# Kernel optimization log

Measured on AMD Instinct MI355X. Metric: run time of the kernel, lower is better.

Reference implementation:

```python
import jax, jax.numpy as jnp
import numpy as np
from jax import lax

N_BLOCK = 4  # unfold kernel/stride

SOBEL_X = jnp.array([[-1., 0., 1.], [-2., 0., 2.], [-1., 0., 1.]], dtype=jnp.float32)
SOBEL_Y = jnp.array([[-1., -2., -1.], [0., 0., 0.], [1., 2., 1.]], dtype=jnp.float32)


def setup_inputs() -> dict:
    key = jax.random.key(0)
    k1, k2 = jax.random.split(key)
    output = jax.random.normal(k1, (16, 1, 1024, 1024), dtype=jnp.float32)
    target = jax.random.normal(k2, (16, 1, 1024, 1024), dtype=jnp.float32)
    return {"output": output, "target": target}


def _sobel(img, kernel):
    # img: (B,1,H,W); cross-correlation with padding 1 (matches nn.Conv2d)
    return lax.conv_general_dilated(img, kernel[None, None], (1, 1), ((1, 1), (1, 1)))


def _block_var(g, n):
    # g: (B,1,H,W) -> per non-overlapping n x n block variance (unbiased=False)
    B, _, H, W = g.shape
    blocks = g.reshape(B, H // n, n, W // n, n)
    m = blocks.mean(axis=(2, 4))
    m2 = (blocks * blocks).mean(axis=(2, 4))
    return (m2 - m * m).reshape(B, -1)  # (B, (H//n)*(W//n))


def reference(output, target):
    loss = jnp.float32(0.0)
    for kern in (SOBEL_X, SOBEL_Y):
        var_out = _block_var(_sobel(output, kern), N_BLOCK)
        var_tgt = _block_var(_sobel(target, kern), N_BLOCK)
        d = var_out - var_tgt
        loss = loss + jnp.sum(d * d)  # MSELoss(reduction='sum')
    return loss
```

## Files before the change

### kernel.cpp

```cpp
#include <hip/hip_runtime.h>

#define IMG_H 1024
#define IMG_W 1024


struct RowRegs { float4 ma, mb; float la, ra_, lb, rb_; };
struct HAB { float hA[4]; float hB[4]; };

__global__ __launch_bounds__(256) void gvl_main(const float* __restrict__ A,
                                                const float* __restrict__ B,
                                                float* __restrict__ partial) {
    const int t    = threadIdx.x;
    const int wave = (blockIdx.x << 2) | (t >> 6);
    const int lane = t & 63;
    const int img   = wave >> 8;
    const int rem   = wave & 255;
    const int band  = rem >> 2;
    const int strip = rem & 3;
    const int y0    = band << 4;
    const int col0  = (strip << 8) | (lane << 2);

    const float* __restrict__ Ab = A + (size_t)img * (IMG_H * IMG_W);
    const float* __restrict__ Bb = B + (size_t)img * (IMG_H * IMG_W);

    const float mlc = (col0 > 0) ? 1.f : 0.f;
    const float mrc = (col0 + 4 < IMG_W) ? 1.f : 0.f;
    const int xl = (col0 > 0) ? col0 - 1 : 0;
    const int xr = (col0 + 4 < IMG_W) ? col0 + 4 : IMG_W - 1;
    const float zlast = (band == 63) ? 0.f : 1.f;

    auto load_row = [&](int y, RowRegs& R) {
        int yc = y < IMG_H ? y : IMG_H - 1;
        const float* ra = Ab + (size_t)yc * IMG_W;
        const float* rb = Bb + (size_t)yc * IMG_W;
        R.ma  = *reinterpret_cast<const float4*>(ra + col0);
        R.la  = ra[xl];  R.ra_ = ra[xr];
        R.mb  = *reinterpret_cast<const float4*>(rb + col0);
        R.lb  = rb[xl];  R.rb_ = rb[xr];
    };
    auto load_group = [&](RowRegs (&S)[4], int ys) {
#pragma unroll
        for (int r = 0; r < 4; ++r) load_row(ys + r, S[r]);
    };

    auto mk = [&](const float4 m, float l, float r, HAB& o) {
        float w0 = l * mlc, w5 = r * mrc;
        o.hA[0] = m.y - w0;  o.hA[1] = m.z - m.x;
        o.hA[2] = m.w - m.y; o.hA[3] = w5 - m.z;
        o.hB[0] = w0 + 2.f * m.x + m.y;
        o.hB[1] = m.x + 2.f * m.y + m.z;
        o.hB[2] = m.y + 2.f * m.z + m.w;
        o.hB[3] = m.z + 2.f * m.w + w5;
    };

    HAB a2, a1, b2, b1;
    float loss = 0.f;

    auto emit = [&](const HAB& p2, const HAB& p1, const HAB& p0,
                    float& sX, float& sX2, float& sY, float& sY2) {
#pragma unroll
        for (int c = 0; c < 4; ++c) {
            float gx = p2.hA[c] + 2.f * p1.hA[c] + p0.hA[c];
            float gy = p0.hB[c] - p2.hB[c];
            sX += gx; sX2 += gx * gx;
            sY += gy; sY2 += gy * gy;
        }
    };

    auto do_group = [&](const RowRegs (&S)[4], float rm3) {
        float sXa = 0.f, sX2a = 0.f, sYa = 0.f, sY2a = 0.f;
        float sXb = 0.f, sX2b = 0.f, sYb = 0.f, sY2b = 0.f;
#pragma unroll
        for (int r = 0; r < 4; ++r) {
            HAB a0, b0;
            mk(S[r].ma, S[r].la, S[r].ra_, a0);
            mk(S[r].mb, S[r].lb, S[r].rb_, b0);
            if (r == 3) {
#pragma unroll
                for (int c = 0; c < 4; ++c) {
                    a0.hA[c] *= rm3; a0.hB[c] *= rm3;
                    b0.hA[c] *= rm3; b0.hB[c] *= rm3;
                }
            }
            emit(a2, a1, a0, sXa, sX2a, sYa, sY2a);
            emit(b2, b1, b0, sXb, sX2b, sYb, sY2b);
            a2 = a1; a1 = a0; b2 = b1; b1 = b0;
        }
        float mXa = sXa * 0.0625f, mYa = sYa * 0.0625f;
        float vXa = sX2a * 0.0625f - mXa * mXa;
        float vYa = sY2a * 0.0625f - mYa * mYa;
        float mXb = sXb * 0.0625f, mYb = sYb * 0.0625f;
        float vXb = sX2b * 0.0625f - mXb * mXb;
        float vYb = sY2b * 0.0625f - mYb * mYb;
        float dX = vXa - vXb, dY = vYa - vYb;
        loss += dX * dX + dY * dY;
    };

    RowRegs P0, P1, N[4], M[4];
    const bool hasPrev = (band > 0);
    if (hasPrev) load_row(y0 - 1, P0);
    load_row(y0, P1);
    load_group(N, y0 + 1);
    if (hasPrev) {
        mk(P0.ma, P0.la, P0.ra_, a2);
        mk(P0.mb, P0.lb, P0.rb_, b2);
    } else {
#pragma unroll
        for (int c = 0; c < 4; ++c) { a2.hA[c] = a2.hB[c] = 0.f; b2.hA[c] = b2.hB[c] = 0.f; }
    }
    mk(P1.ma, P1.la, P1.ra_, a1);
    mk(P1.mb, P1.lb, P1.rb_, b1);

#pragma unroll
    for (int i = 0; i < 2; ++i) {
        load_group(M, y0 + 8 * i + 5);
        do_group(N, 1.f);
        if (i < 1) load_group(N, y0 + 8 * i + 9);
        do_group(M, (i == 1) ? zlast : 1.f);
    }

#pragma unroll
    for (int off = 32; off > 0; off >>= 1) loss += __shfl_down(loss, off);
    if (lane == 0) partial[wave] = loss;
}

__global__ __launch_bounds__(256) void gvl_final(const float* __restrict__ partial,
                                                 float* __restrict__ out) {
    int t = threadIdx.x;
    float s = 0.f;
#pragma unroll
    for (int i = 0; i < 16; ++i) s += partial[t + (i << 8)];
#pragma unroll
    for (int off = 32; off > 0; off >>= 1) s += __shfl_down(s, off);
    __shared__ float ws[4];
    if ((t & 63) == 0) ws[t >> 6] = s;
    __syncthreads();
    if (t == 0) out[0] = ws[0] + ws[1] + ws[2] + ws[3];
}

extern "C" void kernel_launch(void* const* d_in, const int* in_sizes, int n_in,
                              void* d_out, int out_size, void* d_ws, size_t ws_size,
                              hipStream_t stream) {
    const float* out_img = (const float*)d_in[0];
    const float* tgt_img = (const float*)d_in[1];
    float* partial = (float*)d_ws;
    gvl_main<<<1024, 256, 0, stream>>>(out_img, tgt_img, partial);
    gvl_final<<<1, 256, 0, stream>>>(partial, (float*)d_out);
}
```

Baseline: 30.06 us.

## Use 8-column lanes with shuffle halos and 8-row bands with double-buffered rows

```diff
diff --git a/kernel.cpp b/kernel.cpp
--- a/kernel.cpp
+++ b/kernel.cpp
@@ -4,8 +4,7 @@
 #define IMG_W 1024
 
 
-struct RowRegs { float4 ma, mb; float la, ra_, lb, rb_; };
-struct HAB { float hA[4]; float hB[4]; };
+struct Row { float4 qa0, qa1, qb0, qb1; float ea, eb; };
 
 __global__ __launch_bounds__(256) void gvl_main(const float* __restrict__ A,
                                                 const float* __restrict__ B,
@@ -15,108 +14,114 @@
     const int lane = t & 63;
     const int img   = wave >> 8;
     const int rem   = wave & 255;
-    const int band  = rem >> 2;
-    const int strip = rem & 3;
-    const int y0    = band << 4;
-    const int col0  = (strip << 8) | (lane << 2);
+    const int band  = rem >> 1;
+    const int strip = rem & 1;
+    const int y0    = band << 3;
+    const int c0    = (strip << 9) | (lane << 3);
+    const int ecol  = strip ? 511 : 512;
 
-    const float* __restrict__ Ab = A + (size_t)img * (IMG_H * IMG_W);
-    const float* __restrict__ Bb = B + (size_t)img * (IMG_H * IMG_W);
+    const float* __restrict__ Ab = A + (size_t)img * (size_t)(IMG_H * IMG_W);
+    const float* __restrict__ Bb = B + (size_t)img * (size_t)(IMG_H * IMG_W);
 
-    const float mlc = (col0 > 0) ? 1.f : 0.f;
-    const float mrc = (col0 + 4 < IMG_W) ? 1.f : 0.f;
-    const int xl = (col0 > 0) ? col0 - 1 : 0;
-    const int xr = (col0 + 4 < IMG_W) ? col0 + 4 : IMG_W - 1;
-    const float zlast = (band == 63) ? 0.f : 1.f;
+    const float eLs = strip ? 1.f : 0.f;
+    const float eRs = strip ? 0.f : 1.f;
+    const float maskPrev = (band > 0)    ? 1.f : 0.f;
+    const float zlast    = (band == 127) ? 0.f : 1.f;
 
-    auto load_row = [&](int y, RowRegs& R) {
-        int yc = y < IMG_H ? y : IMG_H - 1;
+    auto load_row = [&](int y, Row& R) {
+        int yc = y < 0 ? 0 : (y > IMG_H - 1 ? IMG_H - 1 : y);
         const float* ra = Ab + (size_t)yc * IMG_W;
         const float* rb = Bb + (size_t)yc * IMG_W;
-        R.ma  = *reinterpret_cast<const float4*>(ra + col0);
-        R.la  = ra[xl];  R.ra_ = ra[xr];
-        R.mb  = *reinterpret_cast<const float4*>(rb + col0);
-        R.lb  = rb[xl];  R.rb_ = rb[xr];
-    };
-    auto load_group = [&](RowRegs (&S)[4], int ys) {
-#pragma unroll
-        for (int r = 0; r < 4; ++r) load_row(ys + r, S[r]);
+        R.qa0 = *reinterpret_cast<const float4*>(ra + c0);
+        R.qa1 = *reinterpret_cast<const float4*>(ra + c0 + 4);
+        R.qb0 = *reinterpret_cast<const float4*>(rb + c0);
+        R.qb1 = *reinterpret_cast<const float4*>(rb + c0 + 4);
+        R.ea  = ra[ecol];
+        R.eb  = rb[ecol];
     };
 
-    auto mk = [&](const float4 m, float l, float r, HAB& o) {
-        float w0 = l * mlc, w5 = r * mrc;
-        o.hA[0] = m.y - w0;  o.hA[1] = m.z - m.x;
-        o.hA[2] = m.w - m.y; o.hA[3] = w5 - m.z;
-        o.hB[0] = w0 + 2.f * m.x + m.y;
-        o.hB[1] = m.x + 2.f * m.y + m.z;
-        o.hB[2] = m.y + 2.f * m.z + m.w;
-        o.hB[3] = m.z + 2.f * m.w + w5;
-    };
+    float aX2[8], aX1[8], aB2[8], aB1[8];
+    float bX2[8], bX1[8], bB2[8], bB1[8];
+    float sX[2][2], sXX[2][2], sY[2][2], sYY[2][2];
+#pragma unroll
+    for (int i = 0; i < 2; ++i)
+#pragma unroll
+        for (int j = 0; j < 2; ++j) { sX[i][j] = sXX[i][j] = sY[i][j] = sYY[i][j] = 0.f; }
 
-    HAB a2, a1, b2, b1;
-    float loss = 0.f;
-
-    auto emit = [&](const HAB& p2, const HAB& p1, const HAB& p0,
-                    float& sX, float& sX2, float& sY, float& sY2) {
+    auto calc_h = [&](const float4 q0, const float4 q1, float e, float m,
+                      float (&hX)[8], float (&hB)[8]) {
+        float lv = __shfl_up(q1.w, 1);
+        float rv = __shfl_down(q0.x, 1);
+        lv = (lane == 0)  ? e * eLs : lv;
+        rv = (lane == 63) ? e * eRs : rv;
+        float w[10] = {lv, q0.x, q0.y, q0.z, q0.w, q1.x, q1.y, q1.z, q1.w, rv};
 #pragma unroll
-        for (int c = 0; c < 4; ++c) {
-            float gx = p2.hA[c] + 2.f * p1.hA[c] + p0.hA[c];
-            float gy = p0.hB[c] - p2.hB[c];
-            sX += gx; sX2 += gx * gx;
-            sY += gy; sY2 += gy * gy;
+        for (int c = 0; c < 8; ++c) {
+            hX[c] = (w[c + 2] - w[c]) * m;
+            hB[c] = (w[c] + 2.f * w[c + 1] + w[c + 2]) * m;
         }
     };
 
-    auto do_group = [&](const RowRegs (&S)[4], float rm3) {
-        float sXa = 0.f, sX2a = 0.f, sYa = 0.f, sY2a = 0.f;
-        float sXb = 0.f, sX2b = 0.f, sYb = 0.f, sY2b = 0.f;
+    auto proc_img = [&](const float4 q0, const float4 q1, float e, float m,
+                        float (&X2)[8], float (&X1)[8], float (&B2)[8], float (&B1)[8],
+                        float (&sXi)[2], float (&sXXi)[2],
+                        float (&sYi)[2], float (&sYYi)[2]) {
+        float lv = __shfl_up(q1.w, 1);
+        float rv = __shfl_down(q0.x, 1);
+        lv = (lane == 0)  ? e * eLs : lv;
+        rv = (lane == 63) ? e * eRs : rv;
+        float w[10] = {lv, q0.x, q0.y, q0.z, q0.w, q1.x, q1.y, q1.z, q1.w, rv};
 #pragma unroll
-        for (int r = 0; r < 4; ++r) {
-            HAB a0, b0;
-            mk(S[r].ma, S[r].la, S[r].ra_, a0);
-            mk(S[r].mb, S[r].lb, S[r].rb_, b0);
-            if (r == 3) {
-#pragma unroll
-                for (int c = 0; c < 4; ++c) {
-                    a0.hA[c] *= rm3; a0.hB[c] *= rm3;
-                    b0.hA[c] *= rm3; b0.hB[c] *= rm3;
-                }
-            }
-            emit(a2, a1, a0, sXa, sX2a, sYa, sY2a);
-            emit(b2, b1, b0, sXb, sX2b, sYb, sY2b);
-            a2 = a1; a1 = a0; b2 = b1; b1 = b0;
+        for (int c = 0; c < 8; ++c) {
+            float hX = (w[c + 2] - w[c]) * m;
+            float hB = (w[c] + 2.f * w[c + 1] + w[c + 2]) * m;
+            float gx = X2[c] + 2.f * X1[c] + hX;
+            float gy = hB - B2[c];
+            const int blk = c >> 2;
+            sXi[blk] += gx;  sXXi[blk] += gx * gx;
+            sYi[blk] += gy;  sYYi[blk] += gy * gy;
+            X2[c] = X1[c];  X1[c] = hX;
+            B2[c] = B1[c];  B1[c] = hB;
         }
-        float mXa = sXa * 0.0625f, mYa = sYa * 0.0625f;
-        float vXa = sX2a * 0.0625f - mXa * mXa;
-        float vYa = sY2a * 0.0625f - mYa * mYa;
-        float mXb = sXb * 0.0625f, mYb = sYb * 0.0625f;
-        float vXb = sX2b * 0.0625f - mXb * mXb;
-        float vYb = sY2b * 0.0625f - mYb * mYb;
-        float dX = vXa - vXb, dY = vYa - vYb;
-        loss += dX * dX + dY * dY;
     };
 
-    RowRegs P0, P1, N[4], M[4];
-    const bool hasPrev = (band > 0);
-    if (hasPrev) load_row(y0 - 1, P0);
-    load_row(y0, P1);
-    load_group(N, y0 + 1);
-    if (hasPrev) {
-        mk(P0.ma, P0.la, P0.ra_, a2);
-        mk(P0.mb, P0.lb, P0.rb_, b2);
-    } else {
+    float loss = 0.f;
+    auto finalize = [&]() {
 #pragma unroll
-        for (int c = 0; c < 4; ++c) { a2.hA[c] = a2.hB[c] = 0.f; b2.hA[c] = b2.hB[c] = 0.f; }
-    }
-    mk(P1.ma, P1.la, P1.ra_, a1);
-    mk(P1.mb, P1.lb, P1.rb_, b1);
+        for (int j = 0; j < 2; ++j) {
+            float mXa = sX[0][j] * 0.0625f, mYa = sY[0][j] * 0.0625f;
+            float vXa = sXX[0][j] * 0.0625f - mXa * mXa;
+            float vYa = sYY[0][j] * 0.0625f - mYa * mYa;
+            float mXb = sX[1][j] * 0.0625f, mYb = sY[1][j] * 0.0625f;
+            float vXb = sXX[1][j] * 0.0625f - mXb * mXb;
+            float vYb = sYY[1][j] * 0.0625f - mYb * mYb;
+            float dX = vXa - vXb, dY = vYa - vYb;
+            loss += dX * dX + dY * dY;
+#pragma unroll
+            for (int i = 0; i < 2; ++i) { sX[i][j] = sXX[i][j] = sY[i][j] = sYY[i][j] = 0.f; }
+        }
+    };
+
+    Row Rm, R0, Rb0, Rb1;
+    load_row(y0 - 1, Rm);
+    load_row(y0,     R0);
+    load_row(y0 + 1, Rb0);
+    calc_h(Rm.qa0, Rm.qa1, Rm.ea, maskPrev, aX2, aB2);
+    calc_h(Rm.qb0, Rm.qb1, Rm.eb, maskPrev, bX2, bB2);
+    calc_h(R0.qa0, R0.qa1, R0.ea, 1.f, aX1, aB1);
+    calc_h(R0.qb0, R0.qb1, R0.eb, 1.f, bX1, bB1);
 
 #pragma unroll
-    for (int i = 0; i < 2; ++i) {
-        load_group(M, y0 + 8 * i + 5);
-        do_group(N, 1.f);
-        if (i < 1) load_group(N, y0 + 8 * i + 9);
-        do_group(M, (i == 1) ? zlast : 1.f);
+    for (int k = 0; k < 8; ++k) {
+        Row& cur = (k & 1) ? Rb1 : Rb0;
+        Row& nxt = (k & 1) ? Rb0 : Rb1;
+        if (k < 7) load_row(y0 + 2 + k, nxt);
+        const float m = (k == 7) ? zlast : 1.f;
+        proc_img(cur.qa0, cur.qa1, cur.ea, m, aX2, aX1, aB2, aB1,
+                 sX[0], sXX[0], sY[0], sYY[0]);
+        proc_img(cur.qb0, cur.qb1, cur.eb, m, bX2, bX1, bB2, bB1,
+                 sX[1], sXX[1], sY[1], sYY[1]);
+        if ((k & 3) == 3) finalize();
     }
 
 #pragma unroll
```

Result: slower. 31.23 us (+3.9%).
